# Kernel tuning notes

Measured on AMD Instinct MI355X. Metric: run time of the kernel, lower is better.

Reference implementation:

```python
import jax, jax.numpy as jnp
import numpy as np

B, S, HID = 2, 2048, 2048
H, D, KV = 16, 128, 4          # heads, head_dim, kv heads
REP = H // KV                  # GQA repeat factor
THETA = 10000.0


def setup_inputs() -> dict:
    key = jax.random.key(0)
    ks = jax.random.split(key, 12)
    query = jax.random.normal(ks[0], (B, S, HID), jnp.float32)
    k_in = jax.random.normal(ks[1], (B, S, HID), jnp.float32)
    v_in = jax.random.normal(ks[2], (B, S, HID), jnp.float32)
    # additive causal mask: 0 on/below diag, -10000 above
    causal = jnp.tril(jnp.ones((S, S), jnp.float32))
    mask = jnp.broadcast_to((1.0 - causal) * -10000.0, (B, 1, S, S))
    # rotary tables (cos/sin of freqs_cis), shape [S, D//2]
    inv_freq = 1.0 / (THETA ** (jnp.arange(0, D, 2, dtype=jnp.float32) / D))
    ang = jnp.outer(jnp.arange(S, dtype=jnp.float32), inv_freq)
    freqs_cos, freqs_sin = jnp.cos(ang), jnp.sin(ang)
    sd = 0.02
    Wq = jax.random.normal(ks[3], (HID, H * D), jnp.float32) * sd
    bq = jnp.zeros((H * D,), jnp.float32)
    Wk = jax.random.normal(ks[4], (HID, KV * D), jnp.float32) * sd
    bk = jnp.zeros((KV * D,), jnp.float32)
    Wv = jax.random.normal(ks[5], (HID, KV * D), jnp.float32) * sd
    bv = jnp.zeros((KV * D,), jnp.float32)
    Wo = jax.random.normal(ks[6], (H * D, HID), jnp.float32) * sd
    bo = jnp.zeros((HID,), jnp.float32)
    return {"query": query, "key": k_in, "value": v_in, "mask": mask,
            "freqs_cos": freqs_cos, "freqs_sin": freqs_sin,
            "Wq": Wq, "bq": bq, "Wk": Wk, "bk": bk,
            "Wv": Wv, "bv": bv, "Wo": Wo, "bo": bo}


def _rope(x, cos, sin):
    # x: [B,S,h,D]; pairs adjacent dims as complex (view_as_complex)
    xr = x.reshape(*x.shape[:-1], D // 2, 2)
    xe, xo = xr[..., 0], xr[..., 1]
    c = cos[None, :, None, :]
    s = sin[None, :, None, :]
    re = xe * c - xo * s
    im = xe * s + xo * c
    return jnp.stack([re, im], axis=-1).reshape(x.shape)


def reference(query, key, value, mask, freqs_cos, freqs_sin,
              Wq, bq, Wk, bk, Wv, bv, Wo, bo):
    q = (query @ Wq + bq).reshape(B, S, H, D)
    k = (key @ Wk + bk).reshape(B, S, KV, D)
    v = (value @ Wv + bv).reshape(B, S, KV, D)
    # repeat_kv: torch.repeat_interleave along head dim
    k = jnp.repeat(k, REP, axis=2)
    v = jnpp_repeat = jnp.repeat(v, REP, axis=2)
    q = _rope(q, freqs_cos, freqs_sin)
    k = _rope(k, freqs_cos, freqs_sin)
    q = q.transpose(0, 2, 1, 3)  # [B,H,S,D]
    k = k.transpose(0, 2, 1, 3)
    v = v.transpose(0, 2, 1, 3)
    scores = jnp.einsum('bhqd,bhkd->bhqk', q, k) / jnp.sqrt(jnp.float32(D))
    scores = scores + mask
    probs = jax.nn.softmax(scores, axis=-1)
    ctx = jnp.einsum('bhqk,bhkd->bhqd', probs, v)
    ctx = ctx.transpose(0, 2, 1, 3).reshape(B, S, H * D)
    return ctx @ Wo + bo
```

## Files before the change

kernel.cpp:

```cpp
#include <hip/hip_runtime.h>
#include <stdint.h>

#define BB 2
#define SS 2048
#define HID 2048
#define NH 16
#define DD 128
#define NKV 4

typedef unsigned short u16;
typedef __attribute__((ext_vector_type(8))) short short8;
typedef __attribute__((ext_vector_type(4))) float f32x4;

#if __has_builtin(__builtin_amdgcn_exp2f)
#define EXP2(x) __builtin_amdgcn_exp2f(x)
#else
#define EXP2(x) exp2f(x)
#endif

__device__ __forceinline__ u16 f2bf(float x) {
    union { float f; unsigned u; } v; v.f = x;
    unsigned u = v.u;
    return (u16)((u + 0x7FFFu + ((u >> 16) & 1u)) >> 16);
}

__device__ __forceinline__ void async_lds16(const void* g, void* l) {
    __builtin_amdgcn_global_load_lds(
        (const __attribute__((address_space(1))) void*)(uintptr_t)g,
        (__attribute__((address_space(3))) void*)(uintptr_t)l,
        16, 0, 0);
}

__global__ __launch_bounds__(256) void k_prep(const float* __restrict__ query,
                                              const float* __restrict__ key,
                                              const float* __restrict__ value,
                                              const float* __restrict__ Wq,
                                              const float* __restrict__ Wk,
                                              const float* __restrict__ Wv,
                                              const float* __restrict__ Wo,
                                              u16* __restrict__ qbf,
                                              u16* __restrict__ kbf,
                                              u16* __restrict__ vbf,
                                              u16* __restrict__ Wt,
                                              u16* __restrict__ Wot) {
    __shared__ float tile[32][33];
    int x = blockIdx.x;
    if (x < 24576) {
        const float* in; u16* out;
        if (x < 8192)       { in = query; out = qbf; }
        else if (x < 16384) { in = key;   out = kbf; x -= 8192; }
        else                { in = value; out = vbf; x -= 16384; }
        const int i = x * 256 + threadIdx.x;
        float4 v = ((const float4*)in)[i];
        uint2 o;
        o.x = (unsigned)f2bf(v.x) | ((unsigned)f2bf(v.y) << 16);
        o.y = (unsigned)f2bf(v.z) | ((unsigned)f2bf(v.w) << 16);
        ((uint2*)out)[i] = o;
        return;
    }
    const int v_ = x - 24576;
    const int ty = v_ / 160;
    const int xt = v_ - ty * 160;
    const float* src; u16* dst; int N, n0;
    if (xt < 64)      { src = Wq; dst = Wt;                          N = 2048; n0 = xt * 32; }
    else if (xt < 80) { src = Wk; dst = Wt + (size_t)2048 * 2048;    N = 512;  n0 = (xt - 64) * 32; }
    else if (xt < 96) { src = Wv; dst = Wt + (size_t)2560 * 2048;    N = 512;  n0 = (xt - 80) * 32; }
    else              { src = Wo; dst = Wot;                         N = 2048; n0 = (xt - 96) * 32; }
    const int k0 = ty * 32;
    const int c = threadIdx.x & 31, r = threadIdx.x >> 5;
#pragma unroll
    for (int i = 0; i < 32; i += 8)
        tile[r + i][c] = src[(size_t)(k0 + r + i) * N + n0 + c];
    __syncthreads();
#pragma unroll
    for (int i = 0; i < 32; i += 8)
        dst[(size_t)(n0 + r + i) * 2048 + k0 + c] = f2bf(tile[c][r + i]);
}

__device__ __forceinline__ void gemm128_loop(const u16* __restrict__ gA,
                                             const u16* __restrict__ gB,
                                             const int K, char* smem,
                                             const int wave, const int lane,
                                             f32x4 (&acc)[4][4]) {
    const int r = lane & 15, q4 = lane >> 4;
    const int wm = (wave & 1) * 64, wn = (wave >> 1) * 64;
    u16* As = (u16*)smem;
    u16* Bs = (u16*)(smem + 32768);

    int aoff[4], boff[4];
#pragma unroll
    for (int i = 0; i < 4; i++) {
        const int ar = wm + i * 16 + r;
        aoff[i] = ar * 64 + ((q4 ^ (ar & 7)) << 3);
        const int br = wn + i * 16 + r;
        boff[i] = br * 64 + ((q4 ^ (br & 7)) << 3);
    }

    const int nt = K >> 6;

#define STG128(buf, T) do {                                                                 \
        _Pragma("unroll")                                                                   \
        for (int i_ = 0; i_ < 4; i_++) {                                                    \
            async_lds16(gA + (size_t)(i_ * 32) * K + (size_t)(T) * 64,                      \
                        smem + (buf) * 16384 + (i_ * 32 + wave * 8) * 128);                 \
            async_lds16(gB + (size_t)(i_ * 32) * K + (size_t)(T) * 64,                      \
                        smem + 32768 + (buf) * 16384 + (i_ * 32 + wave * 8) * 128);         \
        }                                                                                   \
    } while (0)

    STG128(0, 0);

    for (int t = 0; t < nt; t++) {
        const int cur = t & 1;
        asm volatile("s_waitcnt vmcnt(0)" ::: "memory");
        __syncthreads();
        if (t + 1 < nt) STG128(cur ^ 1, t + 1);

        const u16* Ab = As + cur * 8192;
        const u16* Bb = Bs + cur * 8192;
        short8 Af[4][2], Bf[4][2];
#pragma unroll
        for (int i = 0; i < 4; i++) {
            Af[i][0] = *(const short8*)(Ab + aoff[i]);
            Af[i][1] = *(const short8*)(Ab + (aoff[i] ^ 32));
            Bf[i][0] = *(const short8*)(Bb + boff[i]);
            Bf[i][1] = *(const short8*)(Bb + (boff[i] ^ 32));
        }
        __builtin_amdgcn_s_setprio(1);
#pragma unroll
        for (int kk = 0; kk < 2; kk++)
#pragma unroll
            for (int i = 0; i < 4; i++)
#pragma unroll
                for (int j = 0; j < 4; j++)
                    acc[i][j] = __builtin_amdgcn_mfma_f32_16x16x32_bf16(Af[i][kk], Bf[j][kk], acc[i][j], 0, 0, 0);
        __builtin_amdgcn_s_setprio(0);
    }
#undef STG128
}

__global__ __launch_bounds__(256, 2) void k_gemm_qkv(const u16* __restrict__ qbf,
                                                     const u16* __restrict__ kbf,
                                                     const u16* __restrict__ vbf,
                                                     const u16* __restrict__ Wt,
                                                     const float* __restrict__ bq,
                                                     const float* __restrict__ bk,
                                                     const float* __restrict__ bv,
                                                     const float* __restrict__ fc,
                                                     const float* __restrict__ fs,
                                                     u16* __restrict__ qro,
                                                     u16* __restrict__ kro,
                                                     u16* __restrict__ vtr) {
    __shared__ char smem[65536];
    const int tid = threadIdx.x;
    const int lane = tid & 63, wave = tid >> 6;
    const int r = lane & 15, q4 = lane >> 4;
    const int wm = (wave & 1) * 64, wn = (wave >> 1) * 64;

    const int linear = blockIdx.y * 24 + blockIdx.x;
    const int nb = (linear & 7) * 96 + (linear >> 3);
    const int bn = nb % 24;
    const int bm = (nb / 24) * 128;

    const u16* A = (bn < 16) ? qbf : (bn < 20) ? kbf : vbf;

    const int srow = wave * 8 + (lane >> 3);
    const int c0 = ((lane & 7) ^ (lane >> 3)) * 8;
    const u16* gA = A  + (size_t)(bm + srow) * 2048 + c0;
    const u16* gB = Wt + (size_t)(bn * 128 + srow) * 2048 + c0;

    f32x4 acc[4][4] = {};
    gemm128_loop(gA, gB, 2048, smem, wave, lane, acc);

    __syncthreads();

    float* Ep = (float*)smem;
    if (bn < 20) {
        const bool isQ = (bn < 16);
        const float qsc = isQ ? 0.08838834764831845f * 1.4426950408889634f : 1.0f;
        const float* bias = isQ ? bq : bk;
        const int head = isQ ? bn : (bn - 16);
        u16* base = isQ ? qro : kro;
        const int nheads = isQ ? NH : NKV;

        float* ep = Ep + wave * 1280;
        const int rowg = bm + wm + lane;
        const int s = rowg & 2047, bidx = rowg >> 11;
        const float* fcp0 = fc + s * 64;
        const float* fsp0 = fs + s * 64;

#pragma unroll
        for (int j = 0; j < 4; j++) {
            const float bcol = bias[head * 128 + wn + j * 16 + r];
#pragma unroll
            for (int i = 0; i < 4; i++)
#pragma unroll
                for (int g = 0; g < 4; g++)
                    ep[(i * 16 + q4 * 4 + g) * 20 + r] = acc[i][j][g] + bcol;
            float4 x0 = *(float4*)(ep + lane * 20 + 0);
            float4 x1 = *(float4*)(ep + lane * 20 + 4);
            float4 x2 = *(float4*)(ep + lane * 20 + 8);
            float4 x3 = *(float4*)(ep + lane * 20 + 12);
            const int d0 = wn + j * 16;
            const int ii0 = d0 >> 1;
            float4 ca = *(const float4*)(fcp0 + ii0);
            float4 cb = *(const float4*)(fcp0 + ii0 + 4);
            float4 sa = *(const float4*)(fsp0 + ii0);
            float4 sb = *(const float4*)(fsp0 + ii0 + 4);
            float o[16];
            o[0]  = (x0.x * ca.x - x0.y * sa.x) * qsc;  o[1]  = (x0.x * sa.x + x0.y * ca.x) * qsc;
            o[2]  = (x0.z * ca.y - x0.w * sa.y) * qsc;  o[3]  = (x0.z * sa.y + x0.w * ca.y) * qsc;
            o[4]  = (x1.x * ca.z - x1.y * sa.z) * qsc;  o[5]  = (x1.x * sa.z + x1.y * ca.z) * qsc;
            o[6]  = (x1.z * ca.w - x1.w * sa.w) * qsc;  o[7]  = (x1.z * sa.w + x1.w * ca.w) * qsc;
            o[8]  = (x2.x * cb.x - x2.y * sb.x) * qsc;  o[9]  = (x2.x * sb.x + x2.y * cb.x) * qsc;
            o[10] = (x2.z * cb.y - x2.w * sb.y) * qsc;  o[11] = (x2.z * sb.y + x2.w * cb.y) * qsc;
            o[12] = (x3.x * cb.z - x3.y * sb.z) * qsc;  o[13] = (x3.x * sb.z + x3.y * cb.z) * qsc;
            o[14] = (x3.z * cb.w - x3.w * sb.w) * qsc;  o[15] = (x3.z * sb.w + x3.w * cb.w) * qsc;
            unsigned w0 = (unsigned)f2bf(o[0])  | ((unsigned)f2bf(o[1])  << 16);
            unsigned w1 = (unsigned)f2bf(o[2])  | ((unsigned)f2bf(o[3])  << 16);
            unsigned w2 = (unsigned)f2bf(o[4])  | ((unsigned)f2bf(o[5])  << 16);
            unsigned w3 = (unsigned)f2bf(o[6])  | ((unsigned)f2bf(o[7])  << 16);
            unsigned w4 = (unsigned)f2bf(o[8])  | ((unsigned)f2bf(o[9])  << 16);
            unsigned w5 = (unsigned)f2bf(o[10]) | ((unsigned)f2bf(o[11]) << 16);
            unsigned w6 = (unsigned)f2bf(o[12]) | ((unsigned)f2bf(o[13]) << 16);
            unsigned w7 = (unsigned)f2bf(o[14]) | ((unsigned)f2bf(o[15]) << 16);
            u16* dst = base + (((size_t)(bidx * nheads + head) * SS + s) << 7) + d0;
            *(uint4*)dst = make_uint4(w0, w1, w2, w3);
            *(uint4*)(dst + 8) = make_uint4(w4, w5, w6, w7);
        }
    } else {
#pragma unroll
        for (int j = 0; j < 4; j++) {
            const int col = bn * 128 + wn + j * 16 + r - 2560;
            const int d = col & 127, kv = col >> 7;
            const float bb = bv[col];
#pragma unroll
            for (int i = 0; i < 4; i++) {
                const int row0 = bm + wm + i * 16 + q4 * 4;
                const int s0 = row0 & 2047, b = row0 >> 11;
                uint2 o;
                o.x = (unsigned)f2bf(acc[i][j][0] + bb) | ((unsigned)f2bf(acc[i][j][1] + bb) << 16);
                o.y = (unsigned)f2bf(acc[i][j][2] + bb) | ((unsigned)f2bf(acc[i][j][3] + bb) << 16);
                *(uint2*)(vtr + ((size_t)(b * NKV + kv) * DD + d) * SS + s0) = o;
            }
        }
    }
}

__global__ __launch_bounds__(256, 2) void k_gemm_bt(const u16* __restrict__ A,
                                                    const u16* __restrict__ Bt,
                                                    const float* __restrict__ bias,
                                                    float* __restrict__ C,
                                                    int M, int N, int K) {
    __shared__ char smem[65536];
    const int tid = threadIdx.x;
    const int lane = tid & 63, wave = tid >> 6;
    const int r = lane & 15, q4 = lane >> 4;
    const int wm = (wave & 1) * 64, wn = (wave >> 1) * 64;

    const int linear = blockIdx.y * 16 + blockIdx.x;
    const int nb = (linear & 7) * 64 + (linear >> 3);
    const int bn0 = (nb & 15) * 128;
    const int bm0 = (nb >> 4) * 128;

    const int srow = wave * 8 + (lane >> 3);
    const int c0 = ((lane & 7) ^ (lane >> 3)) * 8;
    const u16* gA = A  + (size_t)(bm0 + srow) * K + c0;
    const u16* gB = Bt + (size_t)(bn0 + srow) * K + c0;

    f32x4 acc[4][4] = {};
    gemm128_loop(gA, gB, K, smem, wave, lane, acc);

#pragma unroll
    for (int j = 0; j < 4; j++) {
        const int col = bn0 + wn + j * 16 + r;
        const float bb = bias[col];
#pragma unroll
        for (int i = 0; i < 4; i++) {
            const int row = bm0 + wm + i * 16 + q4 * 4;
#pragma unroll
            for (int g = 0; g < 4; g++)
                C[(size_t)(row + g) * N + col] = acc[i][j][g] + bb;
        }
    }
}

__global__ __launch_bounds__(256) void k_attn(const u16* __restrict__ Q,
                                              const u16* __restrict__ K_,
                                              const u16* __restrict__ V_,
                                              u16* __restrict__ Ctx) {
    __shared__ u16 Ks[2][64 * 128];
    __shared__ u16 Vs[2][2 * 128 * 32];
    __shared__ u16 Pb[4][32 * 40];

    const int tid = threadIdx.x;
    const int lane = tid & 63, wave = tid >> 6;
    const int bh = blockIdx.x;
    const int b = bh >> 4, h = bh & 15;
    const int kvh = (b << 2) | (h >> 2);
    const int qb = (gridDim.y - 1 - blockIdx.y) * 128;
    const int qcol = lane & 15, q4 = lane >> 4;
    const int qw = qb + wave * 32;

    const u16* Qg = Q + ((size_t)bh * SS + qw + qcol) * DD;
    short8 qfr[2][4];
#pragma unroll
    for (int qi = 0; qi < 2; qi++)
#pragma unroll
        for (int c = 0; c < 4; c++)
            qfr[qi][c] = *(const short8*)(Qg + qi * 16 * DD + c * 32 + q4 * 8);

    const u16* Kg = K_ + (size_t)kvh * SS * DD;
    const u16* Vg = V_ + (size_t)kvh * DD * SS;

    const int krow = tid >> 4;
    const int kchunk = (tid & 15) ^ (krow & 7);
    const int vd = tid >> 2;
    const int vchunk = (tid & 3) ^ ((vd >> 1) & 3);

    const int nt = (qb + 128) >> 6;
    const int kmax = (nt - 1) * 64;

    f32x4 lacc[2] = {};
    f32x4 oacc[2][8] = {};

    const short8 ones = {0x3F80, 0x3F80, 0x3F80, 0x3F80, 0x3F80, 0x3F80, 0x3F80, 0x3F80};
    u16* pb = &Pb[wave][0];
    unsigned* pb32 = (unsigned*)pb;

#define STAGE_KV(T, BUF) do {                                                                   \
        const int kb_ = min((T) * 64, kmax);                                                    \
        async_lds16(Kg + (size_t)(kb_ + krow) * DD + kchunk * 8,        &Ks[BUF][0] + wave * 512);        \
        async_lds16(Kg + (size_t)(kb_ + 16 + krow) * DD + kchunk * 8,   &Ks[BUF][0] + 2048 + wave * 512); \
        async_lds16(Kg + (size_t)(kb_ + 32 + krow) * DD + kchunk * 8,   &Ks[BUF][0] + 4096 + wave * 512); \
        async_lds16(Kg + (size_t)(kb_ + 48 + krow) * DD + kchunk * 8,   &Ks[BUF][0] + 6144 + wave * 512); \
        async_lds16(Vg + (size_t)vd * SS + kb_ + vchunk * 8,            &Vs[BUF][0] + wave * 512);        \
        async_lds16(Vg + (size_t)vd * SS + kb_ + 32 + vchunk * 8,       &Vs[BUF][0] + 4096 + wave * 512); \
        async_lds16(Vg + (size_t)(vd + 64) * SS + kb_ + vchunk * 8,     &Vs[BUF][0] + 2048 + wave * 512); \
        async_lds16(Vg + (size_t)(vd + 64) * SS + kb_ + 32 + vchunk * 8,&Vs[BUF][0] + 6144 + wave * 512); \
    } while (0)

    STAGE_KV(0, 0);

    for (int t = 0; t < nt; t++) {
        const int kb = t * 64;
        const int cur = t & 1;
        asm volatile("s_waitcnt vmcnt(0)\n\ts_barrier" ::: "memory");
        if (t + 1 < nt) STAGE_KV(t + 1, cur ^ 1);

#pragma unroll
        for (int hh = 0; hh < 2; hh++) {
            const int kbh = kb + hh * 32;
            if (kbh <= qw + 31) {
                const u16* Ksc = &Ks[cur][hh * 32 * 128];
                const u16* Vsc = &Vs[cur][hh * 4096];

                f32x4 sc[2][2] = {};
                __builtin_amdgcn_s_setprio(1);
#pragma unroll
                for (int kt = 0; kt < 2; kt++) {
                    const int kr = kt * 16 + qcol;
#pragma unroll
                    for (int c = 0; c < 4; c++) {
                        short8 kf = *(const short8*)(Ksc + kr * 128 + (((c * 4 + q4) ^ (kr & 7)) << 3));
                        sc[kt][0] = __builtin_amdgcn_mfma_f32_16x16x32_bf16(kf, qfr[0][c], sc[kt][0], 0, 0, 0);
                        sc[kt][1] = __builtin_amdgcn_mfma_f32_16x16x32_bf16(kf, qfr[1][c], sc[kt][1], 0, 0, 0);
                    }
                }
                __builtin_amdgcn_s_setprio(0);

                if (kbh + 32 > qw) {
#pragma unroll
                    for (int kt = 0; kt < 2; kt++)
#pragma unroll
                        for (int qi = 0; qi < 2; qi++)
#pragma unroll
                            for (int g = 0; g < 4; g++) {
                                const int key = kbh + kt * 16 + q4 * 4 + g;
                                if (key > qw + qi * 16 + qcol) sc[kt][qi][g] = -1e30f;
                            }
                }

                const unsigned sel = 0x07060302u;
#pragma unroll
                for (int qi = 0; qi < 2; qi++) {
                    float p0 = EXP2(sc[0][qi][0]), p1 = EXP2(sc[0][qi][1]);
                    float p2 = EXP2(sc[0][qi][2]), p3 = EXP2(sc[0][qi][3]);
                    float p4 = EXP2(sc[1][qi][0]), p5 = EXP2(sc[1][qi][1]);
                    float p6 = EXP2(sc[1][qi][2]), p7 = EXP2(sc[1][qi][3]);
                    unsigned pk0 = __builtin_amdgcn_perm(__float_as_uint(p1), __float_as_uint(p0), sel);
                    unsigned pk1 = __builtin_amdgcn_perm(__float_as_uint(p3), __float_as_uint(p2), sel);
                    unsigned pk2 = __builtin_amdgcn_perm(__float_as_uint(p5), __float_as_uint(p4), sel);
                    unsigned pk3 = __builtin_amdgcn_perm(__float_as_uint(p7), __float_as_uint(p6), sel);
                    const int row = qi * 16 + qcol;
                    *(uint2*)(pb32 + row * 20 + 2 * q4)     = make_uint2(pk0, pk1);
                    *(uint2*)(pb32 + row * 20 + 8 + 2 * q4) = make_uint2(pk2, pk3);
                }

                short8 pf0 = *(const short8*)(pb + qcol * 40 + q4 * 8);
                short8 pf1 = *(const short8*)(pb + (16 + qcol) * 40 + q4 * 8);

                __builtin_amdgcn_s_setprio(1);
                lacc[0] = __builtin_amdgcn_mfma_f32_16x16x32_bf16(ones, pf0, lacc[0], 0, 0, 0);
                lacc[1] = __builtin_amdgcn_mfma_f32_16x16x32_bf16(ones, pf1, lacc[1], 0, 0, 0);
#pragma unroll
                for (int dt = 0; dt < 8; dt++) {
                    const int vr = dt * 16 + qcol;
                    short8 vfr = *(const short8*)(Vsc + vr * 32 + ((q4 ^ ((vr >> 1) & 3)) << 3));
                    oacc[0][dt] = __builtin_amdgcn_mfma_f32_16x16x32_bf16(vfr, pf0, oacc[0][dt], 0, 0, 0);
                    oacc[1][dt] = __builtin_amdgcn_mfma_f32_16x16x32_bf16(vfr, pf1, oacc[1][dt], 0, 0, 0);
                }
                __builtin_amdgcn_s_setprio(0);
            }
        }
    }
#undef STAGE_KV

#pragma unroll
    for (int qi = 0; qi < 2; qi++) {
        const float inv = 1.0f / lacc[qi][0];
        u16* outp = Ctx + ((size_t)b * SS + qw + qi * 16 + qcol) * (NH * DD) + h * DD;
#pragma unroll
        for (int dt = 0; dt < 8; dt++) {
            unsigned lo = (unsigned)f2bf(oacc[qi][dt][0] * inv) | ((unsigned)f2bf(oacc[qi][dt][1] * inv) << 16);
            unsigned hi = (unsigned)f2bf(oacc[qi][dt][2] * inv) | ((unsigned)f2bf(oacc[qi][dt][3] * inv) << 16);
            *(uint2*)(outp + dt * 16 + q4 * 4) = make_uint2(lo, hi);
        }
    }
}

extern "C" void kernel_launch(void* const* d_in, const int* in_sizes, int n_in,
                              void* d_out, int out_size, void* d_ws, size_t ws_size,
                              hipStream_t stream) {
    const float* query = (const float*)d_in[0];
    const float* key   = (const float*)d_in[1];
    const float* value = (const float*)d_in[2];
    const float* fc    = (const float*)d_in[4];
    const float* fs    = (const float*)d_in[5];
    const float* Wq    = (const float*)d_in[6];
    const float* bq    = (const float*)d_in[7];
    const float* Wk    = (const float*)d_in[8];
    const float* bk    = (const float*)d_in[9];
    const float* Wv    = (const float*)d_in[10];
    const float* bv    = (const float*)d_in[11];
    const float* Wo    = (const float*)d_in[12];
    const float* bo    = (const float*)d_in[13];
    float* out = (float*)d_out;

    char* w = (char*)d_ws;
    u16* qbf = (u16*)(w);
    u16* kbf = (u16*)(w + 16777216);
    u16* vbf = (u16*)(w + 33554432);
    u16* Wt  = (u16*)(w + 50331648);
    u16* Wot = (u16*)(w + 62914560);
    u16* qro = (u16*)(w + 71303168);
    u16* kro = (u16*)(w + 88080384);
    u16* vtr = (u16*)(w + 92274688);
    u16* ctx = (u16*)(w + 96468992);

    k_prep<<<34816, 256, 0, stream>>>(query, key, value, Wq, Wk, Wv, Wo,
                                      qbf, kbf, vbf, Wt, Wot);
    k_gemm_qkv<<<dim3(24, 32), 256, 0, stream>>>(qbf, kbf, vbf, Wt, bq, bk, bv,
                                                 fc, fs, qro, kro, vtr);
    k_attn<<<dim3(32, 16), 256, 0, stream>>>(qro, kro, vtr, ctx);
    k_gemm_bt<<<dim3(16, 32), 256, 0, stream>>>(ctx, Wot, bo, out, 4096, 2048, 2048);
}
```

Baseline: 364.6 us.

## Switch GEMM mainloop to triple-buffered K=32 stages with smaller LDS footprint

Reworks the shared GEMM mainloop from double-buffered K=64 tiles to a three-stage ring of K=32 tiles. It uses partial vmcnt waits so two future loads stay in flight, with a new XOR swizzle for the 64-byte rows. LDS per block drops from 64KB to 48KB and launch bounds rise to 3 blocks per CU, aiming to hide global-load latency and raise occupancy. The cost is more barriers per unit of K work, fewer MFMAs between syncs, and possible register pressure at the higher occupancy target.

```diff
diff --git a/kernel.cpp b/kernel.cpp
--- a/kernel.cpp
+++ b/kernel.cpp
@@ -85,61 +85,64 @@
     const int r = lane & 15, q4 = lane >> 4;
     const int wm = (wave & 1) * 64, wn = (wave >> 1) * 64;
     u16* As = (u16*)smem;
-    u16* Bs = (u16*)(smem + 32768);
+    u16* Bs = (u16*)(smem + 24576);
 
     int aoff[4], boff[4];
 #pragma unroll
     for (int i = 0; i < 4; i++) {
         const int ar = wm + i * 16 + r;
-        aoff[i] = ar * 64 + ((q4 ^ (ar & 7)) << 3);
+        aoff[i] = ar * 32 + ((q4 ^ ((r >> 1) & 3)) << 3);
         const int br = wn + i * 16 + r;
-        boff[i] = br * 64 + ((q4 ^ (br & 7)) << 3);
-    }
-
-    const int nt = K >> 6;
-
-#define STG128(buf, T) do {                                                                 \
-        _Pragma("unroll")                                                                   \
-        for (int i_ = 0; i_ < 4; i_++) {                                                    \
-            async_lds16(gA + (size_t)(i_ * 32) * K + (size_t)(T) * 64,                      \
-                        smem + (buf) * 16384 + (i_ * 32 + wave * 8) * 128);                 \
-            async_lds16(gB + (size_t)(i_ * 32) * K + (size_t)(T) * 64,                      \
-                        smem + 32768 + (buf) * 16384 + (i_ * 32 + wave * 8) * 128);         \
-        }                                                                                   \
+        boff[i] = br * 32 + ((q4 ^ ((r >> 1) & 3)) << 3);
+    }
+
+    const int nt = K >> 5;
+
+#define STG32(buf, T) do {                                                                   \
+        async_lds16(gA + (size_t)(wave * 16) * K + (size_t)(T) * 32,                         \
+                    smem + (buf) * 8192 + (wave * 16) * 64);                                 \
+        async_lds16(gA + (size_t)(64 + wave * 16) * K + (size_t)(T) * 32,                    \
+                    smem + (buf) * 8192 + (64 + wave * 16) * 64);                            \
+        async_lds16(gB + (size_t)(wave * 16) * K + (size_t)(T) * 32,                         \
+                    smem + 24576 + (buf) * 8192 + (wave * 16) * 64);                         \
+        async_lds16(gB + (size_t)(64 + wave * 16) * K + (size_t)(T) * 32,                    \
+                    smem + 24576 + (buf) * 8192 + (64 + wave * 16) * 64);                    \
     } while (0)
 
-    STG128(0, 0);
-
+    STG32(0, 0);
+    STG32(1, 1);
+
+    int cur = 0;
     for (int t = 0; t < nt; t++) {
-        const int cur = t & 1;
-        asm volatile("s_waitcnt vmcnt(0)" ::: "memory");
-        __syncthreads();
-        if (t + 1 < nt) STG128(cur ^ 1, t + 1);
-
-        const u16* Ab = As + cur * 8192;
-        const u16* Bb = Bs + cur * 8192;
-        short8 Af[4][2], Bf[4][2];
+        if (t + 1 < nt) asm volatile("s_waitcnt vmcnt(4)\ns_barrier" ::: "memory");
+        else            asm volatile("s_waitcnt vmcnt(0)\ns_barrier" ::: "memory");
+        if (t + 2 < nt) {
+            int nb = cur + 2; if (nb >= 3) nb -= 3;
+            STG32(nb, t + 2);
+        }
+
+        const u16* Ab = As + cur * 4096;
+        const u16* Bb = Bs + cur * 4096;
+        short8 Af[4], Bf[4];
 #pragma unroll
         for (int i = 0; i < 4; i++) {
-            Af[i][0] = *(const short8*)(Ab + aoff[i]);
-            Af[i][1] = *(const short8*)(Ab + (aoff[i] ^ 32));
-            Bf[i][0] = *(const short8*)(Bb + boff[i]);
-            Bf[i][1] = *(const short8*)(Bb + (boff[i] ^ 32));
+            Af[i] = *(const short8*)(Ab + aoff[i]);
+            Bf[i] = *(const short8*)(Bb + boff[i]);
         }
         __builtin_amdgcn_s_setprio(1);
 #pragma unroll
-        for (int kk = 0; kk < 2; kk++)
-#pragma unroll
-            for (int i = 0; i < 4; i++)
-#pragma unroll
-                for (int j = 0; j < 4; j++)
-                    acc[i][j] = __builtin_amdgcn_mfma_f32_16x16x32_bf16(Af[i][kk], Bf[j][kk], acc[i][j], 0, 0, 0);
+        for (int i = 0; i < 4; i++)
+#pragma unroll
+            for (int j = 0; j < 4; j++)
+                acc[i][j] = __builtin_amdgcn_mfma_f32_16x16x32_bf16(Af[i], Bf[j], acc[i][j], 0, 0, 0);
         __builtin_amdgcn_s_setprio(0);
-    }
-#undef STG128
-}
-
-__global__ __launch_bounds__(256, 2) void k_gemm_qkv(const u16* __restrict__ qbf,
+
+        cur = (cur == 2) ? 0 : cur + 1;
+    }
+#undef STG32
+}
+
+__global__ __launch_bounds__(256, 3) void k_gemm_qkv(const u16* __restrict__ qbf,
                                                      const u16* __restrict__ kbf,
                                                      const u16* __restrict__ vbf,
                                                      const u16* __restrict__ Wt,
@@ -151,7 +154,7 @@
                                                      u16* __restrict__ qro,
                                                      u16* __restrict__ kro,
                                                      u16* __restrict__ vtr) {
-    __shared__ char smem[65536];
+    __shared__ char smem[49152];
     const int tid = threadIdx.x;
     const int lane = tid & 63, wave = tid >> 6;
     const int r = lane & 15, q4 = lane >> 4;
@@ -164,8 +167,8 @@
 
     const u16* A = (bn < 16) ? qbf : (bn < 20) ? kbf : vbf;
 
-    const int srow = wave * 8 + (lane >> 3);
-    const int c0 = ((lane & 7) ^ (lane >> 3)) * 8;
+    const int srow = lane >> 2;
+    const int c0 = ((lane & 3) ^ ((srow >> 1) & 3)) * 8;
     const u16* gA = A  + (size_t)(bm + srow) * 2048 + c0;
     const u16* gB = Wt + (size_t)(bn * 128 + srow) * 2048 + c0;
 
@@ -247,12 +250,12 @@
     }
 }
 
-__global__ __launch_bounds__(256, 2) void k_gemm_bt(const u16* __restrict__ A,
+__global__ __launch_bounds__(256, 3) void k_gemm_bt(const u16* __restrict__ A,
                                                     const u16* __restrict__ Bt,
                                                     const float* __restrict__ bias,
                                                     float* __restrict__ C,
                                                     int M, int N, int K) {
-    __shared__ char smem[65536];
+    __shared__ char smem[49152];
     const int tid = threadIdx.x;
     const int lane = tid & 63, wave = tid >> 6;
     const int r = lane & 15, q4 = lane >> 4;
@@ -263,8 +266,8 @@
     const int bn0 = (nb & 15) * 128;
     const int bm0 = (nb >> 4) * 128;
 
-    const int srow = wave * 8 + (lane >> 3);
-    const int c0 = ((lane & 7) ^ (lane >> 3)) * 8;
+    const int srow = lane >> 2;
+    const int c0 = ((lane & 3) ^ ((srow >> 1) & 3)) * 8;
     const u16* gA = A  + (size_t)(bm0 + srow) * K + c0;
     const u16* gB = Bt + (size_t)(bn0 + srow) * K + c0;
 
```

Result: slower. 374.5 us (+2.7%).
